# Optimization experiments

Measured on AMD Instinct MI355X. Metric: run time of the kernel, lower is better.

The kernel has to match this reference:

```python
import jax, jax.numpy as jnp
import numpy as np

B, L, D, H = 2, 2048, 1024, 16
HD = D // H


def setup_inputs() -> dict:
    key = jax.random.key(0)
    ks = jax.random.split(key, 8)
    x = jax.random.normal(ks[0], (B, L, D), dtype=jnp.float32)
    WQ = jax.random.normal(ks[1], (D, D), dtype=jnp.float32) * 0.02
    bQ = jnp.zeros((D,), dtype=jnp.float32)
    WK = jax.random.normal(ks[2], (D, D), dtype=jnp.float32) * 0.02
    bK = jnp.zeros((D,), dtype=jnp.float32)
    WV = jax.random.normal(ks[3], (D, D), dtype=jnp.float32) * 0.02
    bV = jnp.zeros((D,), dtype=jnp.float32)
    Wc = jax.random.normal(ks[4], (D, D), dtype=jnp.float32) * 0.02  # dense channel-mix matrix [d_out, d_in]
    return {"x": x, "WQ": WQ, "bQ": bQ, "WK": WK, "bK": bK, "WV": WV, "bV": bV, "Wc": Wc}


def reference(x, WQ, bQ, WK, bK, WV, bV, Wc):
    b, l, d = x.shape
    # --- TokenMixWeightGenerator (LOW_RANK): T = softmax(causal(Q K^T / sqrt(hd)))
    q = (x @ WQ.T + bQ).reshape(b, l, H, HD).transpose(0, 2, 1, 3)  # [B,H,L,hd]
    k = (x @ WK.T + bK).reshape(b, l, H, HD).transpose(0, 2, 1, 3)  # [B,H,L,hd]
    scores = jnp.einsum("bhid,bhjd->bhij", q, k) / jnp.sqrt(jnp.float32(HD))
    causal_mask = jnp.tril(jnp.ones((l, l), dtype=bool))  # keep j <= i
    scores = jnp.where(causal_mask, scores, -jnp.inf)
    T = jax.nn.softmax(scores, axis=-1)  # [B,H,L,L] explicit token-mix matrix
    # --- UnifiedFeaturizer (expansion=1): V reshaped per head
    v = (x @ WV.T + bV).reshape(b, l, H, HD).transpose(0, 2, 1, 3)  # [B,H,L,hd]
    # --- Y = C @ (T @ V)
    mixed = jnp.einsum("bhij,bhjd->bhid", T, v)  # [B,H,L,hd]
    mixed = mixed.transpose(0, 2, 1, 3).reshape(b, l, d)  # [B,L,D]
    y = mixed @ Wc.T  # channel mixing: output = input @ W.T
    return y
```

## Files before the change

kernel.cpp:

```cpp
#include <hip/hip_runtime.h>


typedef __bf16 bf16x8 __attribute__((ext_vector_type(8)));
typedef float f32x4 __attribute__((ext_vector_type(4)));
typedef unsigned short us4 __attribute__((ext_vector_type(4)));

#if defined(__has_builtin)
#if __has_builtin(__builtin_amdgcn_global_load_lds)
#define HAS_GLL 1
#endif
#endif
#ifndef HAS_GLL
#define HAS_GLL 0
#endif

__device__ __forceinline__ float bf2f(unsigned short u) {
    union { unsigned int i; float f; } v; v.i = ((unsigned int)u) << 16; return v.f;
}
__device__ __forceinline__ unsigned short f2bf(float f) {
    union { float f; unsigned int i; } v; v.f = f;
    unsigned int r = v.i + 0x7FFFu + ((v.i >> 16) & 1u);
    return (unsigned short)(r >> 16);
}
__device__ __forceinline__ unsigned short f2bf_fast(float f) {
    union { float f; unsigned int i; } v; v.f = f;
    return (unsigned short)((v.i + 0x8000u) >> 16);
}
__device__ __forceinline__ f32x4 mfma16(bf16x8 a, bf16x8 b, f32x4 c) {
    return __builtin_amdgcn_mfma_f32_16x16x32_bf16(a, b, c, 0, 0, 0);
}
__device__ __forceinline__ float clamp4(float v) {
    return fminf(fmaxf(v, -1e4f), 1e4f);
}
union U8 { unsigned short s[8]; bf16x8 v; };

#if HAS_GLL
__device__ __forceinline__ void gl_lds16(const unsigned short* g, unsigned short* l) {
    __builtin_amdgcn_global_load_lds(
        (const __attribute__((address_space(1))) void*)g,
        (__attribute__((address_space(3))) void*)l, 16, 0, 0);
}
#endif


__global__ __launch_bounds__(256) void convert_all(
    const float* __restrict__ x, const float* __restrict__ WQ,
    const float* __restrict__ WK, const float* __restrict__ WV,
    const float* __restrict__ Wc,
    unsigned short* __restrict__ xbf, unsigned short* __restrict__ wbf)
{
    size_t e = ((size_t)blockIdx.x * 256 + threadIdx.x) * 8;
    const float* src; unsigned short* dst; size_t off;
    if (e < 4194304) { src = x; dst = xbf; off = e; }
    else {
        size_t j = e - 4194304; int sel = (int)(j >> 20); off = j & 1048575;
        src = (sel == 0) ? WQ : (sel == 1) ? WK : (sel == 2) ? WV : Wc;
        dst = wbf + (size_t)sel * 1048576;
    }
    f32x4 a = *(const f32x4*)(src + off);
    f32x4 b = *(const f32x4*)(src + off + 4);
    U8 u;
    u.s[0] = f2bf(a[0]); u.s[1] = f2bf(a[1]); u.s[2] = f2bf(a[2]); u.s[3] = f2bf(a[3]);
    u.s[4] = f2bf(b[0]); u.s[5] = f2bf(b[1]); u.s[6] = f2bf(b[2]); u.s[7] = f2bf(b[3]);
    *(bf16x8*)(dst + off) = u.v;
}

__global__ __launch_bounds__(256) void gemm128(
    const unsigned short* __restrict__ A, const unsigned short* __restrict__ Wbase,
    const float* __restrict__ b0, const float* __restrict__ b1, const float* __restrict__ b2,
    void* __restrict__ d0, void* __restrict__ d1, void* __restrict__ d2, int modeBase)
{
    const int z = blockIdx.z;
    const unsigned short* W = Wbase + (size_t)z * 1048576;
    const float* bias = (z == 0) ? b0 : (z == 1) ? b1 : b2;
    void* dst = (z == 0) ? d0 : (z == 1) ? d1 : d2;
    const int mode = modeBase + z;

    __shared__ __align__(16) unsigned short At[128][32];
    __shared__ __align__(16) unsigned short Bt[128][32];

    const int mb = blockIdx.y * 128, nb = blockIdx.x * 128;
    const int tid = threadIdx.x, w = tid >> 6, lane = tid & 63;
    const int wr = w >> 1, wc = w & 1;
    const int col = lane & 15, quad = lane >> 4;

    f32x4 acc[4][4];
    for (int i = 0; i < 4; ++i) for (int j = 0; j < 4; ++j) acc[i][j] = (f32x4){0.f, 0.f, 0.f, 0.f};

#if HAS_GLL
    const unsigned short* ga = A + (size_t)(mb + w * 32 + (lane >> 2)) * 1024 + (lane & 3) * 8;
    const unsigned short* gw = W + (size_t)(nb + w * 32 + (lane >> 2)) * 1024 + (lane & 3) * 8;
    unsigned short* lA0 = &At[w * 32][0];
    unsigned short* lA1 = &At[w * 32 + 16][0];
    unsigned short* lB0 = &Bt[w * 32][0];
    unsigned short* lB1 = &Bt[w * 32 + 16][0];
#else
    const int srow = w * 32 + (lane >> 1);
    const int scol = (lane & 1) * 16;
    const unsigned short* Ab = A + (size_t)(mb + srow) * 1024 + scol;
    const unsigned short* Wb = W + (size_t)(nb + srow) * 1024 + scol;
#endif

    for (int kb = 0; kb < 1024; kb += 32) {
#if HAS_GLL
        gl_lds16(ga + kb, lA0);
        gl_lds16(ga + kb + 16 * 1024, lA1);
        gl_lds16(gw + kb, lB0);
        gl_lds16(gw + kb + 16 * 1024, lB1);
#else
        *(bf16x8*)&At[srow][scol]     = *(const bf16x8*)(Ab + kb);
        *(bf16x8*)&At[srow][scol + 8] = *(const bf16x8*)(Ab + kb + 8);
        *(bf16x8*)&Bt[srow][scol]     = *(const bf16x8*)(Wb + kb);
        *(bf16x8*)&Bt[srow][scol + 8] = *(const bf16x8*)(Wb + kb + 8);
#endif
        __syncthreads();
        bf16x8 a[4], b[4];
        for (int i = 0; i < 4; ++i) a[i] = *(const bf16x8*)&At[wr * 64 + i * 16 + col][quad * 8];
        for (int j = 0; j < 4; ++j) b[j] = *(const bf16x8*)&Bt[wc * 64 + j * 16 + col][quad * 8];
        for (int i = 0; i < 4; ++i)
            for (int j = 0; j < 4; ++j)
                acc[i][j] = mfma16(a[i], b[j], acc[i][j]);
        __syncthreads();
    }

    for (int i = 0; i < 4; ++i) {
        const int mbase = mb + wr * 64 + i * 16 + quad * 4;
        const int bb = mbase >> 11, l = mbase & 2047;
        for (int j = 0; j < 4; ++j) {
            const int n = nb + wc * 64 + j * 16 + col;
            const float bv = bias ? bias[n] : 0.f;
            if (mode == 3) {
                float* o = (float*)dst;
                for (int r = 0; r < 4; ++r)
                    o[(size_t)(mbase + r) * 1024 + n] = clamp4(acc[i][j][r] + bv);
            } else if (mode == 2) {
                const int h = n >> 6, hd = n & 63;
                us4 pk;
                for (int r = 0; r < 4; ++r) pk[r] = f2bf(clamp4(acc[i][j][r] + bv));
                *(us4*)((unsigned short*)dst + (size_t)(bb * 16 + h) * 131072
                        + (size_t)hd * 2048 + l) = pk;
            } else {
                const int h = n >> 6, hd = n & 63;
                unsigned short* o = (unsigned short*)dst + (size_t)(bb * 16 + h) * 131072
                                    + (size_t)l * 64 + hd;
                for (int r = 0; r < 4; ++r)
                    o[(size_t)r * 64] = f2bf(clamp4(acc[i][j][r] + bv));
            }
        }
    }
}

__device__ __forceinline__ void attn_tile_step(
    const bf16x8* __restrict__ kf0, const bf16x8* __restrict__ kf1,
    const bf16x8* __restrict__ vf0, const bf16x8* __restrict__ vf1,
    unsigned short (*__restrict__ Pw)[72],
    bf16x8 aq0, bf16x8 aq1, bf16x8 ones,
    f32x4* __restrict__ oacc, f32x4& lacc,
    bool diag, int col, int quad, int w)
{
    f32x4 s[4];
    for (int t = 0; t < 4; ++t) {
        f32x4 z4 = (f32x4){0.f, 0.f, 0.f, 0.f};
        z4 = mfma16(aq0, kf0[t], z4);
        s[t] = mfma16(aq1, kf1[t], z4);
    }
    for (int t = 0; t < 4; ++t)
        for (int r = 0; r < 4; ++r) {
            float v = s[t][r] * 0.125f;
            if (diag && (t * 16 + col > w * 16 + quad * 4 + r)) v = -1e30f;
            v = fminf(v, 60.f);
            Pw[quad * 4 + r][t * 16 + col] = f2bf_fast(__expf(v));
        }
    bf16x8 ap0 = *(const bf16x8*)&Pw[col][quad * 8];
    bf16x8 ap1 = *(const bf16x8*)&Pw[col][32 + quad * 8];
    lacc = mfma16(ap0, ones, lacc);
    lacc = mfma16(ap1, ones, lacc);
    for (int nt = 0; nt < 4; ++nt) {
        oacc[nt] = mfma16(ap0, vf0[nt], oacc[nt]);
        oacc[nt] = mfma16(ap1, vf1[nt], oacc[nt]);
    }
}

__device__ __forceinline__ void attn_write(
    unsigned short* __restrict__ mixed, int gb, int h, int q0, int col, int quad,
    const f32x4* __restrict__ oacc, f32x4 lacc)
{
    f32x4 inv;
    for (int r = 0; r < 4; ++r) inv[r] = 1.f / lacc[r];
    for (int nt = 0; nt < 4; ++nt)
        for (int r = 0; r < 4; ++r) {
            int qrow = q0 + quad * 4 + r;
            mixed[(size_t)(gb * 2048 + qrow) * 1024 + h * 64 + nt * 16 + col] =
                f2bf(clamp4(oacc[nt][r] * inv[r]));
        }
}

__global__ __launch_bounds__(256) void attn_pair(
    const unsigned short* __restrict__ Q, const unsigned short* __restrict__ K,
    const unsigned short* __restrict__ V, unsigned short* __restrict__ mixed)
{
    const int ca = blockIdx.x, cb = 31 - ca, bh = blockIdx.y;
    const int tid = threadIdx.x, w = tid >> 6, lane = tid & 63;
    const int col = lane & 15, quad = lane >> 4;

    __shared__ __align__(16) unsigned short Kt[64][72];
    __shared__ __align__(16) unsigned short Vt[64][72];
    __shared__ __align__(16) unsigned short Plds[4][16][72];

    const unsigned short* Qb = Q + (size_t)bh * 131072;
    const unsigned short* Kb = K + (size_t)bh * 131072;
    const unsigned short* Vb = V + (size_t)bh * 131072;

    const int qa0 = ca * 64 + w * 16, qb0 = cb * 64 + w * 16;
    bf16x8 aqa0 = *(const bf16x8*)(Qb + (size_t)(qa0 + col) * 64 + quad * 8);
    bf16x8 aqa1 = *(const bf16x8*)(Qb + (size_t)(qa0 + col) * 64 + 32 + quad * 8);
    bf16x8 aqb0 = *(const bf16x8*)(Qb + (size_t)(qb0 + col) * 64 + quad * 8);
    bf16x8 aqb1 = *(const bf16x8*)(Qb + (size_t)(qb0 + col) * 64 + 32 + quad * 8);

    U8 onesu;
    for (int i = 0; i < 8; ++i) onesu.s[i] = 0x3F80;
    const bf16x8 ones = onesu.v;

    f32x4 oa[4], ob[4];
    f32x4 la = (f32x4){0.f, 0.f, 0.f, 0.f}, lb = (f32x4){0.f, 0.f, 0.f, 0.f};
    for (int i = 0; i < 4; ++i) { oa[i] = la; ob[i] = la; }

    const int sr = tid >> 3, sc = (tid & 7) * 8;

    const unsigned short* kp = Kb + (size_t)sr * 64 + sc;
    const unsigned short* vp = Vb + (size_t)sr * 2048 + sc;
    bf16x8 pk0 = *(const bf16x8*)kp, pk1 = *(const bf16x8*)(kp + 32 * 64);
    bf16x8 pv0 = *(const bf16x8*)vp, pv1 = *(const bf16x8*)(vp + 32 * 2048);

    for (int kt = 0; kt <= cb; ++kt) {
        __syncthreads();
        *(bf16x8*)&Kt[sr][sc]      = pk0;
        *(bf16x8*)&Kt[sr + 32][sc] = pk1;
        *(bf16x8*)&Vt[sr][sc]      = pv0;
        *(bf16x8*)&Vt[sr + 32][sc] = pv1;
        __syncthreads();
        if (kt < cb) {
            const int kb2 = (kt + 1) * 64;
            const unsigned short* kp2 = Kb + (size_t)(kb2 + sr) * 64 + sc;
            const unsigned short* vp2 = Vb + (size_t)sr * 2048 + kb2 + sc;
            pk0 = *(const bf16x8*)kp2; pk1 = *(const bf16x8*)(kp2 + 32 * 64);
            pv0 = *(const bf16x8*)vp2; pv1 = *(const bf16x8*)(vp2 + 32 * 2048);
        }
        bf16x8 kf0[4], kf1[4], vf0[4], vf1[4];
        for (int t = 0; t < 4; ++t) {
            kf0[t] = *(const bf16x8*)&Kt[t * 16 + col][quad * 8];
            kf1[t] = *(const bf16x8*)&Kt[t * 16 + col][32 + quad * 8];
            vf0[t] = *(const bf16x8*)&Vt[t * 16 + col][quad * 8];
            vf1[t] = *(const bf16x8*)&Vt[t * 16 + col][32 + quad * 8];
        }
        attn_tile_step(kf0, kf1, vf0, vf1, Plds[w], aqb0, aqb1, ones,
                       ob, lb, kt == cb, col, quad, w);
        if (kt <= ca)
            attn_tile_step(kf0, kf1, vf0, vf1, Plds[w], aqa0, aqa1, ones,
                           oa, la, kt == ca, col, quad, w);
    }

    const int gb = bh >> 4, h = bh & 15;
    attn_write(mixed, gb, h, qa0, col, quad, oa, la);
    attn_write(mixed, gb, h, qb0, col, quad, ob, lb);
}


__device__ __forceinline__ bf16x8 load8(const void* base, size_t eoff, int asF32) {
    if (asF32) {
        const float* p = (const float*)base + eoff;
        f32x4 a = *(const f32x4*)p;
        f32x4 b = *(const f32x4*)(p + 4);
        U8 u;
        u.s[0]=f2bf(a[0]); u.s[1]=f2bf(a[1]); u.s[2]=f2bf(a[2]); u.s[3]=f2bf(a[3]);
        u.s[4]=f2bf(b[0]); u.s[5]=f2bf(b[1]); u.s[6]=f2bf(b[2]); u.s[7]=f2bf(b[3]);
        return u.v;
    }
    return *(const bf16x8*)((const unsigned short*)base + eoff);
}

__global__ void dtype_probe(const unsigned short* __restrict__ x, int* __restrict__ flag) {
    if (threadIdx.x == 0) {
        int c = 0;
        for (int i = 0; i < 128; ++i) {
            int e = (x[2 * i] >> 7) & 0xFF;
            if (e >= 100 && e <= 135) ++c;
        }
        *flag = (c < 64) ? 1 : 0;
    }
}

__global__ __launch_bounds__(256) void gemm_bt(
    const void* __restrict__ Ap, const void* __restrict__ Wp,
    const void* __restrict__ biasp, void* __restrict__ dout,
    unsigned short* __restrict__ wsdst, const int* __restrict__ flag,
    long aOff, long outOff, int mode, int aFlagged)
{
    const int f32 = *flag;
    __shared__ __align__(16) unsigned short At[64][32];
    __shared__ __align__(16) unsigned short Bt[64][32];
    const int mb = blockIdx.y * 64, nb = blockIdx.x * 64;
    const int tid = threadIdx.x;
    const int w = tid >> 6, lane = tid & 63;
    const int wr = w >> 1, wc = w & 1;
    const int col = lane & 15, quad = lane >> 4;
    const int srow = tid >> 2, schunk = (tid & 3) * 8;
    const int aF = aFlagged && f32;

    f32x4 acc[2][2];
    for (int i = 0; i < 2; ++i) for (int j = 0; j < 2; ++j) acc[i][j] = (f32x4){0.f,0.f,0.f,0.f};

    const size_t aBase = (size_t)aOff + (size_t)(mb + srow) * 1024 + schunk;
    const size_t wBase = (size_t)(nb + srow) * 1024 + schunk;

    for (int kb = 0; kb < 1024; kb += 32) {
        *(bf16x8*)(&At[srow][schunk]) = load8(Ap, aBase + kb, aF);
        *(bf16x8*)(&Bt[srow][schunk]) = load8(Wp, wBase + kb, f32);
        __syncthreads();
        bf16x8 a0 = *(const bf16x8*)(&At[wr * 32 + col][quad * 8]);
        bf16x8 a1 = *(const bf16x8*)(&At[wr * 32 + 16 + col][quad * 8]);
        bf16x8 b0 = *(const bf16x8*)(&Bt[wc * 32 + col][quad * 8]);
        bf16x8 b1 = *(const bf16x8*)(&Bt[wc * 32 + 16 + col][quad * 8]);
        acc[0][0] = mfma16(a0, b0, acc[0][0]);
        acc[0][1] = mfma16(a0, b1, acc[0][1]);
        acc[1][0] = mfma16(a1, b0, acc[1][0]);
        acc[1][1] = mfma16(a1, b1, acc[1][1]);
        __syncthreads();
    }

    for (int mi = 0; mi < 2; ++mi) {
        for (int ni = 0; ni < 2; ++ni) {
            int n = nb + wc * 32 + ni * 16 + col;
            float bv = 0.f;
            if (biasp) bv = f32 ? ((const float*)biasp)[n] : bf2f(((const unsigned short*)biasp)[n]);
            for (int r = 0; r < 4; ++r) {
                int m = mb + wr * 32 + mi * 16 + quad * 4 + r;
                float v = clamp4(acc[mi][ni][r] + bv);
                if (mode == 3) {
                    size_t idx = (size_t)outOff + (size_t)m * 1024 + n;
                    if (f32) ((float*)dout)[idx] = v;
                    else     ((unsigned short*)dout)[idx] = f2bf(v);
                } else {
                    int h = n >> 6, hd = n & 63;
                    size_t idx = (mode == 2)
                        ? (size_t)h * 131072 + (size_t)hd * 2048 + m
                        : (size_t)h * 131072 + (size_t)m * 64 + hd;
                    unsigned short* dstp = (mode == 0)
                        ? (unsigned short*)dout + (f32 ? 4194304 : 2097152)
                        : wsdst;
                    dstp[idx] = f2bf(v);
                }
            }
        }
    }
}

__global__ __launch_bounds__(256) void attn_kernel(
    const void* __restrict__ dout, const unsigned short* __restrict__ Kw,
    const unsigned short* __restrict__ Vw, unsigned short* __restrict__ mixed,
    const int* __restrict__ flag)
{
    const int f32 = *flag;
    const int qtile = blockIdx.x;
    const int h = blockIdx.y;
    const int w = threadIdx.x >> 6, lane = threadIdx.x & 63;
    const int col = lane & 15, quad = lane >> 4;

    __shared__ __align__(16) unsigned short Plds[4][16][64];

    const unsigned short* Qs = (const unsigned short*)dout + (f32 ? 4194304 : 2097152);
    const unsigned short* Qb = Qs + (size_t)h * 131072;
    const unsigned short* Kb = Kw + (size_t)h * 131072;
    const unsigned short* Vb = Vw + (size_t)h * 131072;

    const int q0 = qtile * 64 + w * 16;
    bf16x8 aq0 = *(const bf16x8*)(Qb + (size_t)(q0 + col) * 64 + quad * 8);
    bf16x8 aq1 = *(const bf16x8*)(Qb + (size_t)(q0 + col) * 64 + 32 + quad * 8);

    float m_run[4] = {-1e30f, -1e30f, -1e30f, -1e30f};
    float l_run[4] = {0.f, 0.f, 0.f, 0.f};
    f32x4 oacc[4];
    for (int i = 0; i < 4; ++i) oacc[i] = (f32x4){0.f, 0.f, 0.f, 0.f};

    for (int kt = 0; kt <= qtile; ++kt) {
        const int kb = kt * 64;
        f32x4 s[4];
        for (int t = 0; t < 4; ++t) {
            s[t] = (f32x4){0.f, 0.f, 0.f, 0.f};
            bf16x8 bk0 = *(const bf16x8*)(Kb + (size_t)(kb + t * 16 + col) * 64 + quad * 8);
            bf16x8 bk1 = *(const bf16x8*)(Kb + (size_t)(kb + t * 16 + col) * 64 + 32 + quad * 8);
            s[t] = mfma16(aq0, bk0, s[t]);
            s[t] = mfma16(aq1, bk1, s[t]);
        }
        for (int t = 0; t < 4; ++t)
            for (int r = 0; r < 4; ++r) {
                float v = clamp4(s[t][r] * 0.125f);
                if (kt == qtile && (t * 16 + col > w * 16 + quad * 4 + r)) v = -1e30f;
                s[t][r] = v;
            }
        float mt[4];
        for (int r = 0; r < 4; ++r)
            mt[r] = fmaxf(fmaxf(s[0][r], s[1][r]), fmaxf(s[2][r], s[3][r]));
        for (int off = 1; off < 16; off <<= 1)
            for (int r = 0; r < 4; ++r)
                mt[r] = fmaxf(mt[r], __shfl_xor(mt[r], off, 64));
        float alpha[4], rs[4], p[4][4];
        for (int r = 0; r < 4; ++r) {
            float mn = fmaxf(m_run[r], mt[r]);
            alpha[r] = __expf(m_run[r] - mn);
            m_run[r] = mn;
        }
        for (int t = 0; t < 4; ++t)
            for (int r = 0; r < 4; ++r)
                p[t][r] = __expf(s[t][r] - m_run[r]);
        for (int r = 0; r < 4; ++r)
            rs[r] = (p[0][r] + p[1][r]) + (p[2][r] + p[3][r]);
        for (int off = 1; off < 16; off <<= 1)
            for (int r = 0; r < 4; ++r)
                rs[r] += __shfl_xor(rs[r], off, 64);
        for (int r = 0; r < 4; ++r)
            l_run[r] = l_run[r] * alpha[r] + rs[r];
        for (int nt = 0; nt < 4; ++nt)
            for (int r = 0; r < 4; ++r)
                oacc[nt][r] *= alpha[r];
        for (int t = 0; t < 4; ++t)
            for (int r = 0; r < 4; ++r)
                Plds[w][quad * 4 + r][t * 16 + col] = f2bf(p[t][r]);
        __syncthreads();
        bf16x8 ap0 = *(const bf16x8*)(&Plds[w][col][quad * 8]);
        bf16x8 ap1 = *(const bf16x8*)(&Plds[w][col][32 + quad * 8]);
        for (int nt = 0; nt < 4; ++nt) {
            bf16x8 bv0 = *(const bf16x8*)(Vb + (size_t)(nt * 16 + col) * 2048 + kb + quad * 8);
            bf16x8 bv1 = *(const bf16x8*)(Vb + (size_t)(nt * 16 + col) * 2048 + kb + 32 + quad * 8);
            oacc[nt] = mfma16(ap0, bv0, oacc[nt]);
            oacc[nt] = mfma16(ap1, bv1, oacc[nt]);
        }
        __syncthreads();
    }

    float inv[4];
    for (int r = 0; r < 4; ++r) inv[r] = 1.f / l_run[r];
    for (int nt = 0; nt < 4; ++nt)
        for (int r = 0; r < 4; ++r) {
            int qrow = q0 + quad * 4 + r;
            mixed[(size_t)qrow * 1024 + h * 64 + nt * 16 + col] = f2bf(clamp4(oacc[nt][r] * inv[r]));
        }
}


extern "C" void kernel_launch(void* const* d_in, const int* in_sizes, int n_in,
                              void* d_out, int out_size, void* d_ws, size_t ws_size,
                              hipStream_t stream) {
    (void)in_sizes; (void)n_in; (void)out_size;
    const void* x  = d_in[0];
    const void* WQ = d_in[1]; const void* bQ = d_in[2];
    const void* WK = d_in[3]; const void* bK = d_in[4];
    const void* WV = d_in[5]; const void* bV = d_in[6];
    const void* Wc = d_in[7];

    if (ws_size >= (size_t)32 * 1024 * 1024) {
        unsigned short* wbf   = (unsigned short*)d_ws;
        unsigned short* Kst   = wbf + 4194304;
        unsigned short* VTst  = Kst + 4194304;
        unsigned short* mixed = VTst + 4194304;
        unsigned short* xbf   = (unsigned short*)d_out;
        unsigned short* Qst   = xbf + 4194304;

        convert_all<<<4096, 256, 0, stream>>>(
            (const float*)x, (const float*)WQ, (const float*)WK,
            (const float*)WV, (const float*)Wc, xbf, wbf);

        gemm128<<<dim3(8, 32, 3), 256, 0, stream>>>(
            xbf, wbf, (const float*)bQ, (const float*)bK, (const float*)bV,
            Qst, Kst, VTst, 0);

        attn_pair<<<dim3(16, 32), 256, 0, stream>>>(Qst, Kst, VTst, mixed);

        gemm128<<<dim3(8, 32, 1), 256, 0, stream>>>(
            mixed, wbf + 3145728, nullptr, nullptr, nullptr,
            d_out, nullptr, nullptr, 3);
    } else {
        unsigned short* wsK = (unsigned short*)d_ws;
        unsigned short* wsV = wsK + 2097152;
        unsigned short* wsM = wsV + 2097152;
        int* flag = (int*)((char*)d_ws + 12 * 1024 * 1024);

        dtype_probe<<<1, 64, 0, stream>>>((const unsigned short*)x, flag);

        dim3 gg(16, 32), gb(256);
        for (int b = 0; b < 2; ++b) {
            long xo = (long)b * 2048 * 1024;
            gemm_bt<<<gg, gb, 0, stream>>>(x, WQ, bQ, d_out, nullptr, flag, xo, 0, 0, 1);
            gemm_bt<<<gg, gb, 0, stream>>>(x, WK, bK, d_out, wsK, flag, xo, 0, 1, 1);
            gemm_bt<<<gg, gb, 0, stream>>>(x, WV, bV, d_out, wsV, flag, xo, 0, 2, 1);
            attn_kernel<<<dim3(32, 16), 256, 0, stream>>>(d_out, wsK, wsV, wsM, flag);
            gemm_bt<<<gg, gb, 0, stream>>>(wsM, Wc, nullptr, d_out, nullptr, flag,
                                           0, (long)b * 2048 * 1024, 3, 0);
        }
    }
}
```

Measured before the change: 194.7 us.

## Split causal attention over two key ranges and merge with a combine kernel

Adds an attention kernel that divides each block's key-tile range into two halves along a new grid z dimension. This doubles the number of workgroups, raising occupancy on the many-CU GPU. Each half writes an unnormalised partial output in bf16 plus its row sums. A new elementwise kernel then adds the two partials and divides by the total sum. The cost is extra global traffic for the partial buffers, an additional kernel launch, and some precision loss from storing unnormalised partials in bf16. The original single-pass kernel is kept as a fallback when the workspace is too small.

```diff
diff --git a/kernel.cpp b/kernel.cpp
--- a/kernel.cpp
+++ b/kernel.cpp
@@ -195,6 +195,118 @@
         }
 }
 
+__device__ __forceinline__ void attn_write_partial(
+    unsigned short* __restrict__ po, float* __restrict__ pl,
+    int gb, int h, int q0, int col, int quad,
+    const f32x4* __restrict__ oacc, f32x4 lacc)
+{
+    for (int nt = 0; nt < 4; ++nt)
+        for (int r = 0; r < 4; ++r) {
+            int qrow = q0 + quad * 4 + r;
+            po[(size_t)(gb * 2048 + qrow) * 1024 + h * 64 + nt * 16 + col] =
+                f2bf(clamp4(oacc[nt][r]));
+        }
+    if (col == 0)
+        for (int r = 0; r < 4; ++r) {
+            int qrow = q0 + quad * 4 + r;
+            pl[(size_t)(gb * 2048 + qrow) * 16 + h] = lacc[r];
+        }
+}
+
+__global__ __launch_bounds__(256) void attn_split(
+    const unsigned short* __restrict__ Q, const unsigned short* __restrict__ K,
+    const unsigned short* __restrict__ V,
+    unsigned short* __restrict__ poBase, float* __restrict__ plBase)
+{
+    const int ca = blockIdx.x, cb = 31 - ca, bh = blockIdx.y, z = blockIdx.z;
+    const int h0end = (cb + 2) >> 1;
+    const int k0 = z ? h0end : 0;
+    const int k1 = z ? (cb + 1) : h0end;
+    unsigned short* po = poBase + (size_t)z * 4194304;
+    float* pl = plBase + (size_t)z * 65536;
+
+    const int tid = threadIdx.x, w = tid >> 6, lane = tid & 63;
+    const int col = lane & 15, quad = lane >> 4;
+
+    __shared__ __align__(16) unsigned short Kt[64][72];
+    __shared__ __align__(16) unsigned short Vt[64][72];
+    __shared__ __align__(16) unsigned short Plds[4][16][72];
+
+    const unsigned short* Qb = Q + (size_t)bh * 131072;
+    const unsigned short* Kb = K + (size_t)bh * 131072;
+    const unsigned short* Vb = V + (size_t)bh * 131072;
+
+    const int qa0 = ca * 64 + w * 16, qb0 = cb * 64 + w * 16;
+    bf16x8 aqa0 = *(const bf16x8*)(Qb + (size_t)(qa0 + col) * 64 + quad * 8);
+    bf16x8 aqa1 = *(const bf16x8*)(Qb + (size_t)(qa0 + col) * 64 + 32 + quad * 8);
+    bf16x8 aqb0 = *(const bf16x8*)(Qb + (size_t)(qb0 + col) * 64 + quad * 8);
+    bf16x8 aqb1 = *(const bf16x8*)(Qb + (size_t)(qb0 + col) * 64 + 32 + quad * 8);
+
+    U8 onesu;
+    for (int i = 0; i < 8; ++i) onesu.s[i] = 0x3F80;
+    const bf16x8 ones = onesu.v;
+
+    f32x4 oa[4], ob[4];
+    f32x4 la = (f32x4){0.f, 0.f, 0.f, 0.f}, lb = (f32x4){0.f, 0.f, 0.f, 0.f};
+    for (int i = 0; i < 4; ++i) { oa[i] = la; ob[i] = la; }
+
+    const int sr = tid >> 3, sc = (tid & 7) * 8;
+
+    const unsigned short* kp = Kb + (size_t)(k0 * 64 + sr) * 64 + sc;
+    const unsigned short* vp = Vb + (size_t)sr * 2048 + k0 * 64 + sc;
+    bf16x8 pk0 = *(const bf16x8*)kp, pk1 = *(const bf16x8*)(kp + 32 * 64);
+    bf16x8 pv0 = *(const bf16x8*)vp, pv1 = *(const bf16x8*)(vp + 32 * 2048);
+
+    for (int kt = k0; kt < k1; ++kt) {
+        __syncthreads();
+        *(bf16x8*)&Kt[sr][sc]      = pk0;
+        *(bf16x8*)&Kt[sr + 32][sc] = pk1;
+        *(bf16x8*)&Vt[sr][sc]      = pv0;
+        *(bf16x8*)&Vt[sr + 32][sc] = pv1;
+        __syncthreads();
+        if (kt + 1 < k1) {
+            const int kb2 = (kt + 1) * 64;
+            const unsigned short* kp2 = Kb + (size_t)(kb2 + sr) * 64 + sc;
+            const unsigned short* vp2 = Vb + (size_t)sr * 2048 + kb2 + sc;
+            pk0 = *(const bf16x8*)kp2; pk1 = *(const bf16x8*)(kp2 + 32 * 64);
+            pv0 = *(const bf16x8*)vp2; pv1 = *(const bf16x8*)(vp2 + 32 * 2048);
+        }
+        bf16x8 kf0[4], kf1[4], vf0[4], vf1[4];
+        for (int t = 0; t < 4; ++t) {
+            kf0[t] = *(const bf16x8*)&Kt[t * 16 + col][quad * 8];
+            kf1[t] = *(const bf16x8*)&Kt[t * 16 + col][32 + quad * 8];
+            vf0[t] = *(const bf16x8*)&Vt[t * 16 + col][quad * 8];
+            vf1[t] = *(const bf16x8*)&Vt[t * 16 + col][32 + quad * 8];
+        }
+        attn_tile_step(kf0, kf1, vf0, vf1, Plds[w], aqb0, aqb1, ones,
+                       ob, lb, kt == cb, col, quad, w);
+        if (kt <= ca)
+            attn_tile_step(kf0, kf1, vf0, vf1, Plds[w], aqa0, aqa1, ones,
+                           oa, la, kt == ca, col, quad, w);
+    }
+
+    const int gb = bh >> 4, h = bh & 15;
+    attn_write_partial(po, pl, gb, h, qa0, col, quad, oa, la);
+    attn_write_partial(po, pl, gb, h, qb0, col, quad, ob, lb);
+}
+
+__global__ __launch_bounds__(256) void attn_combine(
+    unsigned short* __restrict__ mixed, const unsigned short* __restrict__ po1,
+    const float* __restrict__ pl0, const float* __restrict__ pl1)
+{
+    size_t e = ((size_t)blockIdx.x * 256 + threadIdx.x) * 8;
+    const int row = (int)(e >> 10);
+    const int h = ((int)(e >> 6)) & 15;
+    const size_t li = (size_t)row * 16 + h;
+    const float inv = 1.f / (pl0[li] + pl1[li]);
+    U8 ua, ub, uo;
+    ua.v = *(const bf16x8*)(mixed + e);
+    ub.v = *(const bf16x8*)(po1 + e);
+    for (int i = 0; i < 8; ++i)
+        uo.s[i] = f2bf(clamp4((bf2f(ua.s[i]) + bf2f(ub.s[i])) * inv));
+    *(bf16x8*)(mixed + e) = uo.v;
+}
+
 __global__ __launch_bounds__(256) void attn_pair(
     const unsigned short* __restrict__ Q, const unsigned short* __restrict__ K,
     const unsigned short* __restrict__ V, unsigned short* __restrict__ mixed)
@@ -458,11 +570,15 @@
     const void* WV = d_in[5]; const void* bV = d_in[6];
     const void* Wc = d_in[7];
 
+    const size_t NEED_SPLIT = (size_t)40 * 1024 * 1024 + 512 * 1024;
+
     if (ws_size >= (size_t)32 * 1024 * 1024) {
         unsigned short* wbf   = (unsigned short*)d_ws;
         unsigned short* Kst   = wbf + 4194304;
         unsigned short* VTst  = Kst + 4194304;
         unsigned short* mixed = VTst + 4194304;
+        unsigned short* po1   = mixed + 4194304;
+        float* pl             = (float*)(po1 + 4194304);
         unsigned short* xbf   = (unsigned short*)d_out;
         unsigned short* Qst   = xbf + 4194304;
 
@@ -474,7 +590,12 @@
             xbf, wbf, (const float*)bQ, (const float*)bK, (const float*)bV,
             Qst, Kst, VTst, 0);
 
-        attn_pair<<<dim3(16, 32), 256, 0, stream>>>(Qst, Kst, VTst, mixed);
+        if (ws_size >= NEED_SPLIT) {
+            attn_split<<<dim3(16, 32, 2), 256, 0, stream>>>(Qst, Kst, VTst, mixed, pl);
+            attn_combine<<<2048, 256, 0, stream>>>(mixed, po1, pl, pl + 65536);
+        } else {
+            attn_pair<<<dim3(16, 32), 256, 0, stream>>>(Qst, Kst, VTst, mixed);
+        }
 
         gemm128<<<dim3(8, 32, 1), 256, 0, stream>>>(
             mixed, wbf + 3145728, nullptr, nullptr, nullptr,
```

Measured after the change: 201.6 us. 1.04x slower.
